# Optimization experiments

Hardware: AMD Instinct MI355X
Metric: run time of the kernel (lower is better)

## Reference

```python
import jax, jax.numpy as jnp
import numpy as np

N_NODES = 50000


def gcn_conv(x, W, b, src, dst, n_nodes):
    """PyG GCNConv: add self-loops, symmetric norm, linear, scatter-add, bias."""
    h = x @ W  # [N, out]
    # degree with self-loops: deg[i] = 1 + (# edges with dst == i)
    deg = 1.0 + jax.ops.segment_sum(jnp.ones_like(dst, dtype=h.dtype), dst,
                                    num_segments=n_nodes)
    dinv = jax.lax.rsqrt(deg)  # deg^{-1/2}
    # per-edge norm for non-self-loop edges
    norm = dinv[src] * dinv[dst]  # [E]
    agg = jax.ops.segment_sum(h[src] * norm[:, None], dst,
                              num_segments=n_nodes)
    # self-loop contribution: dinv[i]*dinv[i]*h[i] = h[i]/deg[i]
    agg = agg + h * (dinv * dinv)[:, None]
    return agg + b


def setup_inputs() -> dict:
    key = jax.random.key(0)
    ks = jax.random.split(key, 6)
    x = jax.random.normal(ks[0], (N_NODES, 512), dtype=jnp.float32)
    edge_index = jax.random.randint(ks[1], (2, 800000), 0, N_NODES,
                                    dtype=jnp.int64)
    W1 = jax.random.normal(ks[2], (512, 256), dtype=jnp.float32) * (512 ** -0.5)
    b1 = jnp.zeros((256,), dtype=jnp.float32)
    W2 = jax.random.normal(ks[3], (256, 256), dtype=jnp.float32) * (256 ** -0.5)
    b2 = jnp.zeros((256,), dtype=jnp.float32)
    W3 = jax.random.normal(ks[4], (256, 64), dtype=jnp.float32) * (256 ** -0.5)
    b3 = jnp.zeros((64,), dtype=jnp.float32)
    return {"x": x, "edge_index": edge_index, "W1": W1, "b1": b1,
            "W2": W2, "b2": b2, "W3": W3, "b3": b3}


def reference(x, edge_index, W1, b1, W2, b2, W3, b3):
    src, dst = edge_index[0], edge_index[1]
    n = x.shape[0]
    h = gcn_conv(x, W1, b1, src, dst, n)
    h = jax.nn.relu(h)  # dropout is a no-op in eval mode
    h = gcn_conv(h, W2, b2, src, dst, n)
    h = jax.nn.relu(h)
    h = gcn_conv(h, W3, b3, src, dst, n)
    # faithful to the original: softmax then log_softmax
    h = jax.nn.softmax(h, axis=1)
    return jax.nn.log_softmax(h, axis=1)
```

## Files before the change

kernel.cpp:

```cpp
#include <hip/hip_runtime.h>
#include <cstdint>
#include <cstddef>

typedef float  f32x4  __attribute__((ext_vector_type(4)));
typedef float  f32x2  __attribute__((ext_vector_type(2)));

__device__ __forceinline__ unsigned int f2fp8x4(float a, float b, float c, float d) {
  int v = __builtin_amdgcn_cvt_pk_fp8_f32(a, b, 0, false);
  v = __builtin_amdgcn_cvt_pk_fp8_f32(c, d, v, true);
  return (unsigned int)v;
}
__device__ __forceinline__ unsigned char f2fp8(float f) {
  return (unsigned char)(__builtin_amdgcn_cvt_pk_fp8_f32(f, f, 0, false) & 0xff);
}
__device__ __forceinline__ void fp8x8_to_f32(uint2 d, float* f) {
  f32x2 a = __builtin_amdgcn_cvt_pk_f32_fp8((int)d.x, false);
  f32x2 b = __builtin_amdgcn_cvt_pk_f32_fp8((int)d.x, true);
  f32x2 c = __builtin_amdgcn_cvt_pk_f32_fp8((int)d.y, false);
  f32x2 e = __builtin_amdgcn_cvt_pk_f32_fp8((int)d.y, true);
  f[0] = a.x; f[1] = a.y; f[2] = b.x; f[3] = b.y;
  f[4] = c.x; f[5] = c.y; f[6] = e.x; f[7] = e.y;
}
__device__ __forceinline__ void fp8x4_to_f32(unsigned int d, float* f) {
  f32x2 a = __builtin_amdgcn_cvt_pk_f32_fp8((int)d, false);
  f32x2 b = __builtin_amdgcn_cvt_pk_f32_fp8((int)d, true);
  f[0] = a.x; f[1] = a.y; f[2] = b.x; f[3] = b.y;
}
__device__ __forceinline__ void fp8x16_to_f32(uint4 d, float* f) {
  uint2 lo; lo.x = d.x; lo.y = d.y;
  uint2 hi; hi.x = d.z; hi.y = d.w;
  fp8x8_to_f32(lo, f);
  fp8x8_to_f32(hi, f + 8);
}

__device__ __forceinline__ void async_copy16(const void* g, void* l) {
  __builtin_amdgcn_global_load_lds(
      (const __attribute__((address_space(1))) unsigned int*)g,
      (__attribute__((address_space(3))) unsigned int*)l, 16, 0, 0);
}

#define NN 50000
#define MPAD 50048
#define SCAN_BLOCKS 196

#define XB_BLOCKS 6256
#define WB_BLOCKS 52

#define GEMM1_BLOCKS 782
#define COUNT_BLOCKS 3125

__global__ __launch_bounds__(256) void gcn_prep_k(
    const float* __restrict__ X, unsigned char* __restrict__ x8,
    const float* __restrict__ W1, const float* __restrict__ W2,
    const float* __restrict__ W3,
    unsigned char* __restrict__ W1T8, unsigned char* __restrict__ W2T8,
    unsigned char* __restrict__ W3T8, int* __restrict__ cnt) {
  int b = blockIdx.x;
  if (b < SCAN_BLOCKS) {
    int ii = b * 256 + threadIdx.x;
    if (ii < NN) cnt[ii] = 0;
  }
  if (b < XB_BLOCKS) {
    int idx16 = (b * 256 + threadIdx.x) * 16;
    int row = idx16 >> 9;
    uint4 o;
    if (row < NN) {
      const float* s = &X[idx16];
      float4 v0 = *(const float4*)s;
      float4 v1 = *(const float4*)(s + 4);
      float4 v2 = *(const float4*)(s + 8);
      float4 v3 = *(const float4*)(s + 12);
      o.x = f2fp8x4(v0.x, v0.y, v0.z, v0.w);
      o.y = f2fp8x4(v1.x, v1.y, v1.z, v1.w);
      o.z = f2fp8x4(v2.x, v2.y, v2.z, v2.w);
      o.w = f2fp8x4(v3.x, v3.y, v3.z, v3.w);
    } else {
      o = uint4{0, 0, 0, 0};
    }
    *(uint4*)&x8[idx16] = o;
  } else {
    int wb = b - XB_BLOCKS;
    if (wb < 32) {
      int idx16 = (wb * 256 + threadIdx.x) * 16;
      int n = idx16 >> 9;
      float f[16];
#pragma unroll
      for (int j = 0; j < 16; j++) f[j] = W1[(size_t)((idx16 & 511) + j) * 256 + n];
      uint4 o;
      o.x = f2fp8x4(f[0], f[1], f[2], f[3]);
      o.y = f2fp8x4(f[4], f[5], f[6], f[7]);
      o.z = f2fp8x4(f[8], f[9], f[10], f[11]);
      o.w = f2fp8x4(f[12], f[13], f[14], f[15]);
      *(uint4*)&W1T8[idx16] = o;
    } else if (wb < 48) {
      int idx16 = ((wb - 32) * 256 + threadIdx.x) * 16;
      int n = idx16 >> 8;
      float f[16];
#pragma unroll
      for (int j = 0; j < 16; j++) f[j] = W2[(size_t)((idx16 & 255) + j) * 256 + n];
      uint4 o;
      o.x = f2fp8x4(f[0], f[1], f[2], f[3]);
      o.y = f2fp8x4(f[4], f[5], f[6], f[7]);
      o.z = f2fp8x4(f[8], f[9], f[10], f[11]);
      o.w = f2fp8x4(f[12], f[13], f[14], f[15]);
      *(uint4*)&W2T8[idx16] = o;
    } else {
      int idx16 = ((wb - 48) * 256 + threadIdx.x) * 16;
      int n = idx16 >> 8;
      float f[16];
#pragma unroll
      for (int j = 0; j < 16; j++) f[j] = W3[(size_t)((idx16 & 255) + j) * 64 + n];
      uint4 o;
      o.x = f2fp8x4(f[0], f[1], f[2], f[3]);
      o.y = f2fp8x4(f[4], f[5], f[6], f[7]);
      o.z = f2fp8x4(f[8], f[9], f[10], f[11]);
      o.w = f2fp8x4(f[12], f[13], f[14], f[15]);
      *(uint4*)&W3T8[idx16] = o;
    }
  }
}

__global__ __launch_bounds__(256) void gcn_gemm1_count_k(
    const unsigned char* __restrict__ A8,
    const unsigned char* __restrict__ Bt8,
    unsigned char* __restrict__ C8,
    const int* __restrict__ dst, int* __restrict__ cnt, int* __restrict__ rank, int E) {
  __shared__ __align__(16) unsigned char lds_a[2][128 * 32];
  __shared__ __align__(16) unsigned char lds_b[2][128 * 32];
  int b = blockIdx.x;
  if (b >= GEMM1_BLOCKS) {
    int e = (b - GEMM1_BLOCKS) * 256 + threadIdx.x;
    if (e < E) rank[e] = atomicAdd(&cnt[dst[e]], 1);
    return;
  }
  const int K = 512, N = 256;
  const int t = threadIdx.x;
  const int wave = t >> 6, lane = t & 63;
  const int wr = wave >> 1, wc = wave & 1;
  const int quad = lane >> 4, lrow = lane & 15;
  const int m0 = (b >> 1) * 128;
  const int n0 = (b & 1) * 128;

  f32x4 acc[4][4] = {};

  auto stage = [&](int buf, int k0) {
    int r = t >> 1, c = (t & 1) * 16;
    async_copy16(&A8[(size_t)(m0 + r) * K + k0 + c], &lds_a[buf][t * 16]);
    async_copy16(&Bt8[(size_t)(n0 + r) * K + k0 + c], &lds_b[buf][t * 16]);
  };
  auto compute = [&](int buf) {
    long af[4], bfr[4];
#pragma unroll
    for (int mt = 0; mt < 4; mt++)
      af[mt] = *(const long*)&lds_a[buf][(wr * 64 + mt * 16 + lrow) * 32 + quad * 8];
#pragma unroll
    for (int nt = 0; nt < 4; nt++)
      bfr[nt] = *(const long*)&lds_b[buf][(wc * 64 + nt * 16 + lrow) * 32 + quad * 8];
#pragma unroll
    for (int mt = 0; mt < 4; mt++)
#pragma unroll
      for (int nt = 0; nt < 4; nt++)
        acc[mt][nt] = __builtin_amdgcn_mfma_f32_16x16x32_fp8_fp8(af[mt], bfr[nt], acc[mt][nt], 0, 0, 0);
  };

  stage(0, 0);
  int curb = 0;
  int k0 = 0;
  for (; k0 + 32 < K; k0 += 32) {
    stage(curb ^ 1, k0 + 32);
    asm volatile("s_waitcnt vmcnt(2)" ::: "memory");
    __builtin_amdgcn_s_barrier();
    asm volatile("" ::: "memory");
    compute(curb);
    asm volatile("" ::: "memory");
    __builtin_amdgcn_s_barrier();
    curb ^= 1;
  }
  asm volatile("s_waitcnt vmcnt(0)" ::: "memory");
  __builtin_amdgcn_s_barrier();
  asm volatile("" ::: "memory");
  compute(curb);

#pragma unroll
  for (int mt = 0; mt < 4; mt++)
#pragma unroll
    for (int nt = 0; nt < 4; nt++)
#pragma unroll
      for (int r = 0; r < 4; r++) {
        int row = m0 + wr * 64 + mt * 16 + quad * 4 + r;
        int col = n0 + wc * 64 + nt * 16 + lrow;
        C8[(size_t)row * N + col] = f2fp8(acc[mt][nt][r]);
      }
}

__global__ __launch_bounds__(256) void gcn_scan_blocks_k(
    const int* __restrict__ cnt, int* __restrict__ blockSum, int nNodes) {
  __shared__ int sw[4];
  int t = threadIdx.x;
  int i = blockIdx.x * 256 + t;
  int v = (i < nNodes) ? cnt[i] : 0;
  for (int off = 32; off > 0; off >>= 1) v += __shfl_down(v, off);
  if ((t & 63) == 0) sw[t >> 6] = v;
  __syncthreads();
  if (t == 0) blockSum[blockIdx.x] = sw[0] + sw[1] + sw[2] + sw[3];
}

__global__ __launch_bounds__(256) void gcn_scan_final_k(
    const int* __restrict__ cnt, const int* __restrict__ blockSum,
    int* __restrict__ rs, float* __restrict__ dinv, int nNodes, int E) {
  __shared__ int sb[256];
  __shared__ int sc[256];
  int t = threadIdx.x;
  int i = blockIdx.x * 256 + t;
  int v = (i < nNodes) ? cnt[i] : 0;
  sb[t] = v;
  int w = (t < SCAN_BLOCKS) ? blockSum[t] : 0;
  sc[t] = w;
  __syncthreads();
  for (int off = 1; off < 256; off <<= 1) {
    int x = (t >= off) ? sb[t - off] : 0;
    int y = (t >= off) ? sc[t - off] : 0;
    __syncthreads();
    sb[t] += x;
    sc[t] += y;
    __syncthreads();
  }
  int base = sc[blockIdx.x] - blockSum[blockIdx.x];
  if (i < nNodes) {
    rs[i] = base + sb[t] - v;
    dinv[i] = rsqrtf(1.0f + (float)v);
  } else if (i < MPAD) {
    dinv[i] = 0.0f;
  }
  if (i == 0) rs[nNodes] = E;
}

__global__ void gcn_scatter_k(const int* __restrict__ src, const int* __restrict__ dst,
                              const int* __restrict__ rank, const int* __restrict__ rs,
                              int* __restrict__ e4, int E) {
  int e = blockIdx.x * 256 + threadIdx.x;
  if (e < E) {
    int d = dst[e];
    e4[rs[d] + rank[e]] = src[e];
  }
}

template<int BN, int WTN>
__global__ __launch_bounds__(256) void gcn_gemm_f8_db_k(
    const unsigned char* __restrict__ A8,
    const unsigned char* __restrict__ Bt8,
    const float* __restrict__ dinv,
    unsigned char* __restrict__ C8,
    int K, int N) {
  static_assert(BN == 128, "db kernel assumes uniform 2 global_load_lds per thread");
  __shared__ __align__(16) unsigned char lds_a[2][128 * 32];
  __shared__ __align__(16) unsigned char lds_b[2][BN * 32];
  const int t = threadIdx.x;
  const int wave = t >> 6, lane = t & 63;
  const int wr = wave >> 1, wc = wave & 1;
  const int quad = lane >> 4, lrow = lane & 15;
  const int m0 = blockIdx.x * 128;
  const int n0 = blockIdx.y * BN;

  f32x4 acc[4][WTN] = {};

  auto stage = [&](int buf, int k0) {
    int r = t >> 1, c = (t & 1) * 16;
    async_copy16(&A8[(size_t)(m0 + r) * K + k0 + c], &lds_a[buf][t * 16]);
    async_copy16(&Bt8[(size_t)(n0 + r) * K + k0 + c], &lds_b[buf][t * 16]);
  };
  auto compute = [&](int buf) {
    long af[4], bfr[WTN];
#pragma unroll
    for (int mt = 0; mt < 4; mt++)
      af[mt] = *(const long*)&lds_a[buf][(wr * 64 + mt * 16 + lrow) * 32 + quad * 8];
#pragma unroll
    for (int nt = 0; nt < WTN; nt++)
      bfr[nt] = *(const long*)&lds_b[buf][(wc * (BN / 2) + nt * 16 + lrow) * 32 + quad * 8];
#pragma unroll
    for (int mt = 0; mt < 4; mt++)
#pragma unroll
      for (int nt = 0; nt < WTN; nt++)
        acc[mt][nt] = __builtin_amdgcn_mfma_f32_16x16x32_fp8_fp8(af[mt], bfr[nt], acc[mt][nt], 0, 0, 0);
  };

  stage(0, 0);
  int curb = 0;
  int k0 = 0;
  for (; k0 + 32 < K; k0 += 32) {
    stage(curb ^ 1, k0 + 32);
    asm volatile("s_waitcnt vmcnt(2)" ::: "memory");
    __builtin_amdgcn_s_barrier();
    asm volatile("" ::: "memory");
    compute(curb);
    asm volatile("" ::: "memory");
    __builtin_amdgcn_s_barrier();
    curb ^= 1;
  }
  asm volatile("s_waitcnt vmcnt(0)" ::: "memory");
  __builtin_amdgcn_s_barrier();
  asm volatile("" ::: "memory");
  compute(curb);

#pragma unroll
  for (int mt = 0; mt < 4; mt++)
#pragma unroll
    for (int r = 0; r < 4; r++) {
      int row = m0 + wr * 64 + mt * 16 + quad * 4 + r;
      float dv = dinv[row];
#pragma unroll
      for (int nt = 0; nt < WTN; nt++) {
        int col = n0 + wc * (BN / 2) + nt * 16 + lrow;
        C8[(size_t)row * N + col] = f2fp8(acc[mt][nt][r] * dv);
      }
    }
}

template<int BN, int WTN>
__global__ __launch_bounds__(256) void gcn_gemm_f8_s_k(
    const unsigned char* __restrict__ A8, const unsigned char* __restrict__ Bt8,
    const float* __restrict__ dinv, unsigned char* __restrict__ C8, int K, int N) {
  __shared__ __align__(16) unsigned char lds_a[128 * 32];
  __shared__ __align__(16) unsigned char lds_b[BN * 32];
  const int t = threadIdx.x;
  const int wave = t >> 6, lane = t & 63;
  const int wr = wave >> 1, wc = wave & 1;
  const int quad = lane >> 4, lrow = lane & 15;
  const int m0 = blockIdx.x * 128;
  const int n0 = blockIdx.y * BN;

  f32x4 acc[4][WTN] = {};

  for (int k0 = 0; k0 < K; k0 += 32) {
    __syncthreads();
    {
      int r = t >> 1, c = (t & 1) * 16;
      async_copy16(&A8[(size_t)(m0 + r) * K + k0 + c], &lds_a[t * 16]);
    }
    for (int q = t; q < BN * 2; q += 256) {
      int r = q >> 1, c = (q & 1) * 16;
      async_copy16(&Bt8[(size_t)(n0 + r) * K + k0 + c], &lds_b[q * 16]);
    }
    __syncthreads();
    long af[4], bfr[WTN];
#pragma unroll
    for (int mt = 0; mt < 4; mt++)
      af[mt] = *(const long*)&lds_a[(wr * 64 + mt * 16 + lrow) * 32 + quad * 8];
#pragma unroll
    for (int nt = 0; nt < WTN; nt++)
      bfr[nt] = *(const long*)&lds_b[(wc * (BN / 2) + nt * 16 + lrow) * 32 + quad * 8];
#pragma unroll
    for (int mt = 0; mt < 4; mt++)
#pragma unroll
      for (int nt = 0; nt < WTN; nt++)
        acc[mt][nt] = __builtin_amdgcn_mfma_f32_16x16x32_fp8_fp8(af[mt], bfr[nt], acc[mt][nt], 0, 0, 0);
  }

#pragma unroll
  for (int mt = 0; mt < 4; mt++)
#pragma unroll
    for (int r = 0; r < 4; r++) {
      int row = m0 + wr * 64 + mt * 16 + quad * 4 + r;
      float dv = dinv[row];
#pragma unroll
      for (int nt = 0; nt < WTN; nt++) {
        int col = n0 + wc * (BN / 2) + nt * 16 + lrow;
        C8[(size_t)row * N + col] = f2fp8(acc[mt][nt][r] * dv);
      }
    }
}

template<int D, int WSRC>
__global__ __launch_bounds__(256) void gcn_agg_relu_k(
    const unsigned char* __restrict__ g8, const int* __restrict__ rs,
    const int* __restrict__ e4, const float* __restrict__ dinv,
    const float* __restrict__ bias, unsigned char* __restrict__ out8, int nNodes) {
  int wave = threadIdx.x >> 6, lane = threadIdx.x & 63;
  int i = blockIdx.x * 4 + wave;
  if (i >= nNodes) return;
  int q = lane >> 4, sub = lane & 15;
  int f0 = sub * 16;
  float di = dinv[i];
  uint4 dself = *(const uint4*)&g8[(size_t)i * D + f0];
  float sv[16];
  fp8x16_to_f32(dself, sv);
  float wself = (q == 0) ? (WSRC ? di : 1.0f) : 0.0f;
  float acc[16];
#pragma unroll
  for (int j = 0; j < 16; j++) acc[j] = sv[j] * wself;

  int e0 = rs[i], e1 = rs[i + 1];
  int nIter = (e1 - e0 + 15) >> 4;
  int e = e0 + q;
  for (int k = 0; k < nIter; k++) {
    int idx[4]; float w[4];
#pragma unroll
    for (int u = 0; u < 4; u++) {
      int ee = e + 4 * u;
      bool v = ee < e1;
      idx[u] = v ? e4[ee] : 0;
      w[u] = v ? (WSRC ? dinv[idx[u]] : 1.0f) : 0.0f;
    }
    uint4 d0 = *(const uint4*)&g8[(size_t)idx[0] * D + f0];
    uint4 d1 = *(const uint4*)&g8[(size_t)idx[1] * D + f0];
    uint4 d2 = *(const uint4*)&g8[(size_t)idx[2] * D + f0];
    uint4 d3 = *(const uint4*)&g8[(size_t)idx[3] * D + f0];
    float r[16];
    fp8x16_to_f32(d0, r);
#pragma unroll
    for (int j = 0; j < 16; j++) acc[j] += r[j] * w[0];
    fp8x16_to_f32(d1, r);
#pragma unroll
    for (int j = 0; j < 16; j++) acc[j] += r[j] * w[1];
    fp8x16_to_f32(d2, r);
#pragma unroll
    for (int j = 0; j < 16; j++) acc[j] += r[j] * w[2];
    fp8x16_to_f32(d3, r);
#pragma unroll
    for (int j = 0; j < 16; j++) acc[j] += r[j] * w[3];
    e += 16;
  }
#pragma unroll
  for (int j = 0; j < 16; j++) {
    acc[j] += __shfl_xor(acc[j], 16);
    acc[j] += __shfl_xor(acc[j], 32);
  }
  if (q == 0) {
    float4 bb0 = *(const float4*)&bias[f0];
    float4 bb1 = *(const float4*)&bias[f0 + 4];
    float4 bb2 = *(const float4*)&bias[f0 + 8];
    float4 bb3 = *(const float4*)&bias[f0 + 12];
    float bv[16] = {bb0.x, bb0.y, bb0.z, bb0.w, bb1.x, bb1.y, bb1.z, bb1.w,
                    bb2.x, bb2.y, bb2.z, bb2.w, bb3.x, bb3.y, bb3.z, bb3.w};
    float r[16];
#pragma unroll
    for (int j = 0; j < 16; j++) {
      float z = di * acc[j] + bv[j];
      r[j] = z > 0.0f ? z : 0.0f;
    }
    uint4 o;
    o.x = f2fp8x4(r[0], r[1], r[2], r[3]);
    o.y = f2fp8x4(r[4], r[5], r[6], r[7]);
    o.z = f2fp8x4(r[8], r[9], r[10], r[11]);
    o.w = f2fp8x4(r[12], r[13], r[14], r[15]);
    *(uint4*)&out8[(size_t)i * D + f0] = o;
  }
}

__global__ __launch_bounds__(256) void gcn_agg_final_k(
    const unsigned char* __restrict__ g8, const int* __restrict__ rs,
    const int* __restrict__ e4, const float* __restrict__ dinv,
    const float* __restrict__ bias, float* __restrict__ out, int nNodes) {
  int wave = threadIdx.x >> 6, lane = threadIdx.x & 63;
  int i = blockIdx.x * 4 + wave;
  if (i >= nNodes) return;
  int qtr = lane >> 4, sub = lane & 15;
  int f0 = sub * 4;
  float di = dinv[i];
  unsigned int dself = *(const unsigned int*)&g8[(size_t)i * 64 + f0];
  float sv[4];
  fp8x4_to_f32(dself, sv);
  float wself = (qtr == 0) ? 1.0f : 0.0f;
  float acc[4];
#pragma unroll
  for (int j = 0; j < 4; j++) acc[j] = sv[j] * wself;

  int e0 = rs[i], e1 = rs[i + 1];
  int nIter = (e1 - e0 + 7) >> 3;
  int e = e0 + qtr;
  for (int k = 0; k < nIter; k++) {
    int idx[2]; float w[2];
#pragma unroll
    for (int u = 0; u < 2; u++) {
      int ee = e + 4 * u;
      bool v = ee < e1;
      idx[u] = v ? e4[ee] : 0;
      w[u] = v ? 1.0f : 0.0f;
    }
    unsigned int d0 = *(const unsigned int*)&g8[(size_t)idx[0] * 64 + f0];
    unsigned int d1 = *(const unsigned int*)&g8[(size_t)idx[1] * 64 + f0];
    float r0[4], r1[4];
    fp8x4_to_f32(d0, r0); fp8x4_to_f32(d1, r1);
#pragma unroll
    for (int j = 0; j < 4; j++)
      acc[j] += r0[j] * w[0] + r1[j] * w[1];
    e += 8;
  }
#pragma unroll
  for (int j = 0; j < 4; j++) {
    acc[j] += __shfl_xor(acc[j], 16);
    acc[j] += __shfl_xor(acc[j], 32);
    acc[j] = di * acc[j] + bias[f0 + j];
  }
  float m = fmaxf(fmaxf(acc[0], acc[1]), fmaxf(acc[2], acc[3]));
#pragma unroll
  for (int off = 8; off > 0; off >>= 1) m = fmaxf(m, __shfl_xor(m, off));
  float ex[4], s = 0.0f;
#pragma unroll
  for (int j = 0; j < 4; j++) { ex[j] = __expf(acc[j] - m); s += ex[j]; }
#pragma unroll
  for (int off = 8; off > 0; off >>= 1) s += __shfl_xor(s, off);
  float rcs = 1.0f / s;
  float p[4], s2 = 0.0f;
#pragma unroll
  for (int j = 0; j < 4; j++) { p[j] = ex[j] * rcs; s2 += __expf(p[j]); }
#pragma unroll
  for (int off = 8; off > 0; off >>= 1) s2 += __shfl_xor(s2, off);
  float ls = __logf(s2);
  if (qtr == 0) {
    float4 o; o.x = p[0] - ls; o.y = p[1] - ls; o.z = p[2] - ls; o.w = p[3] - ls;
    *(float4*)&out[(size_t)i * 64 + f0] = o;
  }
}

extern "C" void kernel_launch(void* const* d_in, const int* in_sizes, int n_in,
                              void* d_out, int out_size, void* d_ws, size_t ws_size,
                              hipStream_t stream) {
  const float* x    = (const float*)d_in[0];
  const int*   eidx = (const int*)d_in[1];
  const float* W1   = (const float*)d_in[2];
  const float* b1   = (const float*)d_in[3];
  const float* W2   = (const float*)d_in[4];
  const float* b2   = (const float*)d_in[5];
  const float* W3   = (const float*)d_in[6];
  const float* b3   = (const float*)d_in[7];
  float* out = (float*)d_out;

  const int E = in_sizes[1] / 2;
  const int* src = eidx;
  const int* dst = eidx + E;

  char* p = (char*)d_ws;
  auto alloc = [&](size_t bytes) -> void* {
    void* r = (void*)p;
    p += (bytes + 255) & ~(size_t)255;
    return r;
  };
  unsigned char*  x8   = (unsigned char*)alloc((size_t)MPAD * 512);
  unsigned char*  g8   = (unsigned char*)alloc((size_t)MPAD * 256);
  unsigned char*  a8   = (unsigned char*)alloc((size_t)MPAD * 256);
  unsigned char*  g83  = (unsigned char*)alloc((size_t)MPAD * 64);
  unsigned char*  W1T8 = (unsigned char*)alloc((size_t)256 * 512);
  unsigned char*  W2T8 = (unsigned char*)alloc((size_t)256 * 256);
  unsigned char*  W3T8 = (unsigned char*)alloc((size_t)64 * 256);
  int*   cnt  = (int*)alloc((size_t)NN * 4);
  int*   rs   = (int*)alloc((size_t)(NN + 1) * 4);
  int*   rank = (int*)alloc((size_t)E * 4);
  float* dinv = (float*)alloc((size_t)MPAD * 4);
  int*   e4   = (int*)alloc((size_t)(E + 64) * 4);
  int*   bsum = (int*)alloc((size_t)SCAN_BLOCKS * 4);

  const int EB = (E + 255) / 256;
  gcn_prep_k<<<XB_BLOCKS + WB_BLOCKS, 256, 0, stream>>>(
      x, x8, W1, W2, W3, W1T8, W2T8, W3T8, cnt);
  gcn_gemm1_count_k<<<GEMM1_BLOCKS + COUNT_BLOCKS, 256, 0, stream>>>(
      x8, W1T8, g8, dst, cnt, rank, E);
  gcn_scan_blocks_k<<<SCAN_BLOCKS, 256, 0, stream>>>(cnt, bsum, NN);
  gcn_scan_final_k<<<SCAN_BLOCKS, 256, 0, stream>>>(cnt, bsum, rs, dinv, NN, E);
  gcn_scatter_k<<<EB, 256, 0, stream>>>(src, dst, rank, rs, e4, E);
  gcn_agg_relu_k<256, 1><<<(NN + 3) / 4, 256, 0, stream>>>(g8, rs, e4, dinv, b1, a8, NN);
  const int MB = MPAD / 128;
  gcn_gemm_f8_db_k<128, 4><<<dim3(MB, 2), 256, 0, stream>>>(a8, W2T8, dinv, g8, 256, 256);
  gcn_agg_relu_k<256, 0><<<(NN + 3) / 4, 256, 0, stream>>>(g8, rs, e4, dinv, b2, a8, NN);
  gcn_gemm_f8_s_k<64, 2><<<dim3(MB, 1), 256, 0, stream>>>(a8, W3T8, dinv, g83, 256, 64);
  gcn_agg_final_k<<<(NN + 3) / 4, 256, 0, stream>>>(g83, rs, e4, dinv, b3, out, NN);

  (void)n_in; (void)out_size; (void)ws_size;
}
```

Baseline: 385.1 us.

## Pad degree counters to separate cache lines and schedule count blocks first

Degree counters are now spaced CSTR=32 ints (128 bytes) apart, so each node's atomic counter sits on its own cache line and atomics on neighbouring nodes stop contending for one line. The fused kernel also puts the edge-count blocks ahead of the GEMM blocks, so the atomics are dispatched first and overlap with the GEMM tiles. In exchange the counter array grows 32x (about 6.4MB), and the scan kernels now read strided memory, one int per 128-byte line.

```diff
diff --git a/kernel.cpp b/kernel.cpp
--- a/kernel.cpp
+++ b/kernel.cpp
@@ -42,6 +42,7 @@
 #define NN 50000
 #define MPAD 50048
 #define SCAN_BLOCKS 196
+#define CSTR 32
 
 #define XB_BLOCKS 6256
 #define WB_BLOCKS 52
@@ -54,11 +55,11 @@
     const float* __restrict__ W1, const float* __restrict__ W2,
     const float* __restrict__ W3,
     unsigned char* __restrict__ W1T8, unsigned char* __restrict__ W2T8,
-    unsigned char* __restrict__ W3T8, int* __restrict__ cnt) {
+    unsigned char* __restrict__ W3T8, int* __restrict__ cntp) {
   int b = blockIdx.x;
   if (b < SCAN_BLOCKS) {
     int ii = b * 256 + threadIdx.x;
-    if (ii < NN) cnt[ii] = 0;
+    if (ii < NN) cntp[(size_t)ii * CSTR] = 0;
   }
   if (b < XB_BLOCKS) {
     int idx16 = (b * 256 + threadIdx.x) * 16;
@@ -120,26 +121,27 @@
   }
 }
 
-__global__ __launch_bounds__(256) void gcn_gemm1_count_k(
+__global__ __launch_bounds__(256) void gcn_count_gemm1_k(
     const unsigned char* __restrict__ A8,
     const unsigned char* __restrict__ Bt8,
     unsigned char* __restrict__ C8,
-    const int* __restrict__ dst, int* __restrict__ cnt, int* __restrict__ rank, int E) {
+    const int* __restrict__ dst, int* __restrict__ cntp, int* __restrict__ rank, int E) {
   __shared__ __align__(16) unsigned char lds_a[2][128 * 32];
   __shared__ __align__(16) unsigned char lds_b[2][128 * 32];
   int b = blockIdx.x;
-  if (b >= GEMM1_BLOCKS) {
-    int e = (b - GEMM1_BLOCKS) * 256 + threadIdx.x;
-    if (e < E) rank[e] = atomicAdd(&cnt[dst[e]], 1);
+  if (b < COUNT_BLOCKS) {
+    int e = b * 256 + threadIdx.x;
+    if (e < E) rank[e] = atomicAdd(&cntp[(size_t)dst[e] * CSTR], 1);
     return;
   }
+  int bg = b - COUNT_BLOCKS;
   const int K = 512, N = 256;
   const int t = threadIdx.x;
   const int wave = t >> 6, lane = t & 63;
   const int wr = wave >> 1, wc = wave & 1;
   const int quad = lane >> 4, lrow = lane & 15;
-  const int m0 = (b >> 1) * 128;
-  const int n0 = (b & 1) * 128;
+  const int m0 = (bg >> 1) * 128;
+  const int n0 = (bg & 1) * 128;
 
   f32x4 acc[4][4] = {};
 
@@ -194,11 +196,11 @@
 }
 
 __global__ __launch_bounds__(256) void gcn_scan_blocks_k(
-    const int* __restrict__ cnt, int* __restrict__ blockSum, int nNodes) {
+    const int* __restrict__ cntp, int* __restrict__ blockSum, int nNodes) {
   __shared__ int sw[4];
   int t = threadIdx.x;
   int i = blockIdx.x * 256 + t;
-  int v = (i < nNodes) ? cnt[i] : 0;
+  int v = (i < nNodes) ? cntp[(size_t)i * CSTR] : 0;
   for (int off = 32; off > 0; off >>= 1) v += __shfl_down(v, off);
   if ((t & 63) == 0) sw[t >> 6] = v;
   __syncthreads();
@@ -206,13 +208,13 @@
 }
 
 __global__ __launch_bounds__(256) void gcn_scan_final_k(
-    const int* __restrict__ cnt, const int* __restrict__ blockSum,
+    const int* __restrict__ cntp, const int* __restrict__ blockSum,
     int* __restrict__ rs, float* __restrict__ dinv, int nNodes, int E) {
   __shared__ int sb[256];
   __shared__ int sc[256];
   int t = threadIdx.x;
   int i = blockIdx.x * 256 + t;
-  int v = (i < nNodes) ? cnt[i] : 0;
+  int v = (i < nNodes) ? cntp[(size_t)i * CSTR] : 0;
   sb[t] = v;
   int w = (t < SCAN_BLOCKS) ? blockSum[t] : 0;
   sc[t] = w;
@@ -543,7 +545,7 @@
   unsigned char*  W1T8 = (unsigned char*)alloc((size_t)256 * 512);
   unsigned char*  W2T8 = (unsigned char*)alloc((size_t)256 * 256);
   unsigned char*  W3T8 = (unsigned char*)alloc((size_t)64 * 256);
-  int*   cnt  = (int*)alloc((size_t)NN * 4);
+  int*   cntp = (int*)alloc((size_t)NN * CSTR * 4);
   int*   rs   = (int*)alloc((size_t)(NN + 1) * 4);
   int*   rank = (int*)alloc((size_t)E * 4);
   float* dinv = (float*)alloc((size_t)MPAD * 4);
@@ -552,11 +554,11 @@
 
   const int EB = (E + 255) / 256;
   gcn_prep_k<<<XB_BLOCKS + WB_BLOCKS, 256, 0, stream>>>(
-      x, x8, W1, W2, W3, W1T8, W2T8, W3T8, cnt);
-  gcn_gemm1_count_k<<<GEMM1_BLOCKS + COUNT_BLOCKS, 256, 0, stream>>>(
-      x8, W1T8, g8, dst, cnt, rank, E);
-  gcn_scan_blocks_k<<<SCAN_BLOCKS, 256, 0, stream>>>(cnt, bsum, NN);
-  gcn_scan_final_k<<<SCAN_BLOCKS, 256, 0, stream>>>(cnt, bsum, rs, dinv, NN, E);
+      x, x8, W1, W2, W3, W1T8, W2T8, W3T8, cntp);
+  gcn_count_gemm1_k<<<COUNT_BLOCKS + GEMM1_BLOCKS, 256, 0, stream>>>(
+      x8, W1T8, g8, dst, cntp, rank, E);
+  gcn_scan_blocks_k<<<SCAN_BLOCKS, 256, 0, stream>>>(cntp, bsum, NN);
+  gcn_scan_final_k<<<SCAN_BLOCKS, 256, 0, stream>>>(cntp, bsum, rs, dinv, NN, E);
   gcn_scatter_k<<<EB, 256, 0, stream>>>(src, dst, rank, rs, e4, E);
   gcn_agg_relu_k<256, 1><<<(NN + 3) / 4, 256, 0, stream>>>(g8, rs, e4, dinv, b1, a8, NN);
   const int MB = MPAD / 128;
```

Result: slower. 396.4 us (+2.9%).

## Merge scan kernels with grid barrier and batch edge counting before GEMM1

Applied to the files above, without the earlier changes.

Replaces the two-kernel degree scan with a single kernel that uses a global atomic spin barrier between the per-block reduction and the final prefix step, removing one launch. The edge-count atomics now run in 512 grid-stride blocks that issue eight loads and atomics per thread, and they are placed before the GEMM1 blocks so they are scheduled first. The grid barrier relies on all 196 blocks being resident at the same time, and its counter is reset in the prep kernel.

```diff
diff --git a/kernel.cpp b/kernel.cpp
--- a/kernel.cpp
+++ b/kernel.cpp
@@ -46,20 +46,22 @@
 #define XB_BLOCKS 6256
 #define WB_BLOCKS 52
 
+#define CNT_BLOCKS 512
+#define CNT_GS (CNT_BLOCKS * 256)
 #define GEMM1_BLOCKS 782
-#define COUNT_BLOCKS 3125
 
 __global__ __launch_bounds__(256) void gcn_prep_k(
     const float* __restrict__ X, unsigned char* __restrict__ x8,
     const float* __restrict__ W1, const float* __restrict__ W2,
     const float* __restrict__ W3,
     unsigned char* __restrict__ W1T8, unsigned char* __restrict__ W2T8,
-    unsigned char* __restrict__ W3T8, int* __restrict__ cnt) {
+    unsigned char* __restrict__ W3T8, int* __restrict__ cnt, int* __restrict__ bar) {
   int b = blockIdx.x;
   if (b < SCAN_BLOCKS) {
     int ii = b * 256 + threadIdx.x;
     if (ii < NN) cnt[ii] = 0;
   }
+  if (b == 0 && threadIdx.x < 8) bar[threadIdx.x] = 0;
   if (b < XB_BLOCKS) {
     int idx16 = (b * 256 + threadIdx.x) * 16;
     int row = idx16 >> 9;
@@ -120,7 +122,7 @@
   }
 }
 
-__global__ __launch_bounds__(256) void gcn_gemm1_count_k(
+__global__ __launch_bounds__(256) void gcn_count_gemm1_k(
     const unsigned char* __restrict__ A8,
     const unsigned char* __restrict__ Bt8,
     unsigned char* __restrict__ C8,
@@ -128,18 +130,35 @@
   __shared__ __align__(16) unsigned char lds_a[2][128 * 32];
   __shared__ __align__(16) unsigned char lds_b[2][128 * 32];
   int b = blockIdx.x;
-  if (b >= GEMM1_BLOCKS) {
-    int e = (b - GEMM1_BLOCKS) * 256 + threadIdx.x;
-    if (e < E) rank[e] = atomicAdd(&cnt[dst[e]], 1);
+  if (b < CNT_BLOCKS) {
+    int e = b * 256 + threadIdx.x;
+    for (; e < E; ) {
+      int ee[8]; bool v[8]; int d[8];
+#pragma unroll
+      for (int k = 0; k < 8; k++) {
+        ee[k] = e + k * CNT_GS;
+        v[k] = ee[k] < E;
+        d[k] = v[k] ? dst[ee[k]] : 0;
+      }
+      int r[8];
+#pragma unroll
+      for (int k = 0; k < 8; k++)
+        if (v[k]) r[k] = atomicAdd(&cnt[d[k]], 1);
+#pragma unroll
+      for (int k = 0; k < 8; k++)
+        if (v[k]) rank[ee[k]] = r[k];
+      e += 8 * CNT_GS;
+    }
     return;
   }
+  int bg = b - CNT_BLOCKS;
   const int K = 512, N = 256;
   const int t = threadIdx.x;
   const int wave = t >> 6, lane = t & 63;
   const int wr = wave >> 1, wc = wave & 1;
   const int quad = lane >> 4, lrow = lane & 15;
-  const int m0 = (b >> 1) * 128;
-  const int n0 = (b & 1) * 128;
+  const int m0 = (bg >> 1) * 128;
+  const int n0 = (bg & 1) * 128;
 
   f32x4 acc[4][4] = {};
 
@@ -193,46 +212,51 @@
       }
 }
 
-__global__ __launch_bounds__(256) void gcn_scan_blocks_k(
-    const int* __restrict__ cnt, int* __restrict__ blockSum, int nNodes) {
-  __shared__ int sw[4];
-  int t = threadIdx.x;
-  int i = blockIdx.x * 256 + t;
-  int v = (i < nNodes) ? cnt[i] : 0;
-  for (int off = 32; off > 0; off >>= 1) v += __shfl_down(v, off);
-  if ((t & 63) == 0) sw[t >> 6] = v;
+__device__ __forceinline__ void gbar(int* bar, int target) {
   __syncthreads();
-  if (t == 0) blockSum[blockIdx.x] = sw[0] + sw[1] + sw[2] + sw[3];
-}
-
-__global__ __launch_bounds__(256) void gcn_scan_final_k(
-    const int* __restrict__ cnt, const int* __restrict__ blockSum,
-    int* __restrict__ rs, float* __restrict__ dinv, int nNodes, int E) {
+  if (threadIdx.x == 0) {
+    __hip_atomic_fetch_add(bar, 1, __ATOMIC_ACQ_REL, __HIP_MEMORY_SCOPE_AGENT);
+    while (__hip_atomic_load(bar, __ATOMIC_ACQUIRE, __HIP_MEMORY_SCOPE_AGENT) < target)
+      __builtin_amdgcn_s_sleep(2);
+  }
+  __syncthreads();
+}
+
+__global__ __launch_bounds__(256) void gcn_scan_k(
+    const int* __restrict__ cnt, int* __restrict__ rs, float* __restrict__ dinv,
+    int* __restrict__ bsum, int* __restrict__ bar, int E) {
   __shared__ int sb[256];
   __shared__ int sc[256];
-  int t = threadIdx.x;
-  int i = blockIdx.x * 256 + t;
-  int v = (i < nNodes) ? cnt[i] : 0;
+  const int t = threadIdx.x, b = blockIdx.x;
+  const int i = b * 256 + t;
+  int v = (i < NN) ? cnt[i] : 0;
   sb[t] = v;
-  int w = (t < SCAN_BLOCKS) ? blockSum[t] : 0;
+  __syncthreads();
+  for (int off = 1; off < 256; off <<= 1) {
+    int x = (t >= off) ? sb[t - off] : 0;
+    __syncthreads();
+    sb[t] += x;
+    __syncthreads();
+  }
+  if (t == 255) bsum[b] = sb[255];
+  gbar(bar, SCAN_BLOCKS);
+  int w = (t < SCAN_BLOCKS) ? bsum[t] : 0;
   sc[t] = w;
   __syncthreads();
   for (int off = 1; off < 256; off <<= 1) {
-    int x = (t >= off) ? sb[t - off] : 0;
     int y = (t >= off) ? sc[t - off] : 0;
     __syncthreads();
-    sb[t] += x;
     sc[t] += y;
     __syncthreads();
   }
-  int base = sc[blockIdx.x] - blockSum[blockIdx.x];
-  if (i < nNodes) {
+  int base = sc[b] - bsum[b];
+  if (i < NN) {
     rs[i] = base + sb[t] - v;
     dinv[i] = rsqrtf(1.0f + (float)v);
   } else if (i < MPAD) {
     dinv[i] = 0.0f;
   }
-  if (i == 0) rs[nNodes] = E;
+  if (i == 0) rs[NN] = E;
 }
 
 __global__ void gcn_scatter_k(const int* __restrict__ src, const int* __restrict__ dst,
@@ -549,14 +573,14 @@
   float* dinv = (float*)alloc((size_t)MPAD * 4);
   int*   e4   = (int*)alloc((size_t)(E + 64) * 4);
   int*   bsum = (int*)alloc((size_t)SCAN_BLOCKS * 4);
+  int*   bar  = (int*)alloc((size_t)8 * 4);
 
   const int EB = (E + 255) / 256;
   gcn_prep_k<<<XB_BLOCKS + WB_BLOCKS, 256, 0, stream>>>(
-      x, x8, W1, W2, W3, W1T8, W2T8, W3T8, cnt);
-  gcn_gemm1_count_k<<<GEMM1_BLOCKS + COUNT_BLOCKS, 256, 0, stream>>>(
+      x, x8, W1, W2, W3, W1T8, W2T8, W3T8, cnt, bar);
+  gcn_count_gemm1_k<<<CNT_BLOCKS + GEMM1_BLOCKS, 256, 0, stream>>>(
       x8, W1T8, g8, dst, cnt, rank, E);
-  gcn_scan_blocks_k<<<SCAN_BLOCKS, 256, 0, stream>>>(cnt, bsum, NN);
-  gcn_scan_final_k<<<SCAN_BLOCKS, 256, 0, stream>>>(cnt, bsum, rs, dinv, NN, E);
+  gcn_scan_k<<<SCAN_BLOCKS, 256, 0, stream>>>(cnt, rs, dinv, bsum, bar, E);
   gcn_scatter_k<<<EB, 256, 0, stream>>>(src, dst, rank, rs, e4, E);
   gcn_agg_relu_k<256, 1><<<(NN + 3) / 4, 256, 0, stream>>>(g8, rs, e4, dinv, b1, a8, NN);
   const int MB = MPAD / 128;
```

Result: slower. 405.6 us (+5.3%).
